# Performance work log

Measured on AMD Instinct MI355X. Metric: run time of the kernel, lower is better.

Reference implementation:

```python
import jax, jax.numpy as jnp
import numpy as np

B = 16384
D = 768           # roberta hidden
SENT = 3          # sentiment features
GRU_IN = D + SENT # 771
H = 128           # memory_dim
FUSION = GRU_IN + H + D  # 1667
E = 7             # num_emotions
S = 65536         # number of (dialog, speaker) memory slots


def setup_inputs() -> dict:
    key = jax.random.key(0)
    ks = jax.random.split(key, 12)
    inp = {
        "h_t": jax.random.normal(ks[0], (B, D), jnp.float32),
        "h_ctx": jax.random.normal(ks[1], (B, D), jnp.float32),
        "sentiment": jax.random.uniform(ks[2], (B, SENT), jnp.float32),
        "slot_ids": jax.random.randint(ks[3], (B,), 0, S, jnp.int32),
        # speaker memory table (gathered/scattered by slot_ids)
        "memory": jax.random.normal(ks[4], (S, H), jnp.float32) * 0.1,
        # GRUCell params (torch layout: rows ordered [r; z; n])
        "W_ih": jax.random.normal(ks[5], (3 * H, GRU_IN), jnp.float32) * 0.02,
        "W_hh": jax.random.normal(ks[6], (3 * H, H), jnp.float32) * 0.02,
        "b_ih": jnp.zeros((3 * H,), jnp.float32),
        "b_hh": jnp.zeros((3 * H,), jnp.float32),
        # heads
        "W_e": jax.random.normal(ks[7], (E, FUSION), jnp.float32) * 0.02,
        "b_e": jnp.zeros((E,), jnp.float32),
        "W_s": jax.random.normal(ks[8], (1, FUSION), jnp.float32) * 0.02,
        "b_s": jnp.zeros((1,), jnp.float32),
    }
    return inp


def _gru_cell(x, h, W_ih, W_hh, b_ih, b_hh):
    # x: [B, GRU_IN], h: [B, H]; torch nn.GRUCell semantics
    gi = x @ W_ih.T + b_ih            # [B, 3H]
    gh = h @ W_hh.T + b_hh            # [B, 3H]
    i_r, i_z, i_n = jnp.split(gi, 3, axis=1)
    h_r, h_z, h_n = jnp.split(gh, 3, axis=1)
    r = jax.nn.sigmoid(i_r + h_r)
    z = jax.nn.sigmoid(i_z + h_z)
    n = jnp.tanh(i_n + r * h_n)
    return (1.0 - z) * n + z * h


def reference(h_t, h_ctx, sentiment, slot_ids, memory, W_ih, W_hh, b_ih, b_hh, W_e, b_e, W_s, b_s):
    h_t_aug = jnp.concatenate([h_t, sentiment], axis=1)      # [B, 771]
    s_t = memory[slot_ids]                                    # gather  [B, H]
    s_new = _gru_cell(h_t_aug, s_t, W_ih, W_hh, b_ih, b_hh)   # [B, H]
    # prediction uses the PRE-update memory s_t (as in the torch loop)
    z_t = jnp.concatenate([h_t_aug, s_t, h_ctx], axis=1)      # [B, 1667] (dropout is identity in eval)
    emotion_logits = z_t @ W_e.T + b_e                        # [B, E]
    shift_logits = (z_t @ W_s.T + b_s)[:, 0]                  # [B]
    # matching the sequential dict updates in the original loop)
    new_memory = memory.at[slot_ids].set(s_new)               # [S, H]
    return emotion_logits, shift_logits, new_memory
```

## Files before the change

### kernel.cpp

```cpp
#include <hip/hip_runtime.h>
#include <hip/hip_bf16.h>

#define B_SZ   16384
#define D_SZ   768
#define H_SZ   128
#define S_SZ   65536
#define E_SZ   7

#define NFR    33
#define NSTEP  53

typedef __attribute__((ext_vector_type(8))) short bf16x8;
typedef __attribute__((ext_vector_type(4))) float f32x4;

#define LD4(p) (*reinterpret_cast<const float4*>(p))
#define MFMA(d, a, b) d = __builtin_amdgcn_mfma_f32_16x16x32_bf16(a, b, d, 0, 0, 0)

#define GLDS(gp, lp) __builtin_amdgcn_global_load_lds(                              \
        (const __attribute__((address_space(1))) unsigned int*)(gp),                \
        (__attribute__((address_space(3))) unsigned int*)(lp), 16, 0, 0)

static __device__ __forceinline__ ushort f2bf(float v) {
    unsigned u = __float_as_uint(v);
    u = (u + 0x7FFFu + ((u >> 16) & 1u)) >> 16;
    return (ushort)u;
}

static __device__ __forceinline__ unsigned pk2(float x, float y) {
    unsigned a = __float_as_uint(x) + 0x8000u;
    unsigned b = __float_as_uint(y) + 0x8000u;
    return __builtin_amdgcn_perm(b, a, 0x07060302);
}

static __device__ __forceinline__ bf16x8 cvt8(float4 a, float4 b) {
    union { unsigned u[4]; bf16x8 v; } r;
    r.u[0] = pk2(a.x, a.y); r.u[1] = pk2(a.z, a.w);
    r.u[2] = pk2(b.x, b.y); r.u[3] = pk2(b.z, b.w);
    return r.v;
}

static __device__ __forceinline__ float w2_value(int n, int k,
    const float* __restrict__ W_ih, const float* __restrict__ W_hh,
    const float* __restrict__ b_ih, const float* __restrict__ b_hh,
    const float* __restrict__ W_e,  const float* __restrict__ b_e,
    const float* __restrict__ W_s,  const float* __restrict__ b_s)
{
    float v = 0.0f;
    if (n < 256) {
        if (k < 768)                        v = W_ih[(size_t)n * 771 + k];
        else if (k < 896)                   v = W_hh[(size_t)n * 128 + (k - 768)];
        else if (k >= 1664 && k < 1667)     v = W_ih[(size_t)n * 771 + 768 + (k - 1664)];
        else if (k == 1667)                 v = b_ih[n] + b_hh[n];
    } else if (n < 384) {
        if (k < 768)                        v = W_ih[(size_t)n * 771 + k];
        else if (k >= 1664 && k < 1667)     v = W_ih[(size_t)n * 771 + 768 + (k - 1664)];
        else if (k == 1667)                 v = b_ih[n];
    } else if (n < 512) {
        int g = n - 128;
        if (k >= 768 && k < 896)            v = W_hh[(size_t)g * 128 + (k - 768)];
        else if (k == 1667)                 v = b_hh[g];
    } else if (n < 520) {
        int e = n - 512;
        const float* Wr = (e < E_SZ) ? (W_e + (size_t)e * 1667) : W_s;
        if (k < 768)                        v = Wr[k];
        else if (k < 896)                   v = Wr[771 + (k - 768)];
        else if (k < 1664)                  v = Wr[899 + (k - 896)];
        else if (k < 1667)                  v = Wr[768 + (k - 1664)];
        else if (k == 1667)                 v = (e < E_SZ) ? b_e[e] : b_s[0];
    }
    return v;
}

__global__ __launch_bounds__(256) void pack_w2f_kernel(
    const float* __restrict__ W_ih, const float* __restrict__ W_hh,
    const float* __restrict__ b_ih, const float* __restrict__ b_hh,
    const float* __restrict__ W_e,  const float* __restrict__ b_e,
    const float* __restrict__ W_s,  const float* __restrict__ b_s,
    ushort* __restrict__ W2f)
{
    int tid = blockIdx.x * 256 + threadIdx.x;
    if (tid >= NFR * NSTEP * 64) return;
    int lane  = tid & 63;
    int kstep = (tid >> 6) % NSTEP;
    int nf    = tid / (NSTEP * 64);
    int n     = nf * 16 + (lane & 15);
    int kbase = kstep * 32 + (lane >> 4) * 8;
    ushort o[8];
#pragma unroll
    for (int j = 0; j < 8; ++j)
        o[j] = f2bf(w2_value(n, kbase + j, W_ih, W_hh, b_ih, b_hh, W_e, b_e, W_s, b_s));
    *reinterpret_cast<uint4*>(W2f + (size_t)tid * 8) = *reinterpret_cast<const uint4*>(o);
}

__global__ __launch_bounds__(256) void winner_kernel(const int* __restrict__ slot_ids,
                                                     int* __restrict__ winner)
{
    int b = blockIdx.x * 256 + threadIdx.x;
    if (b < B_SZ) atomicMax(&winner[slot_ids[b]], b);
}

static __device__ __forceinline__ bf16x8 ldB(const ushort* __restrict__ W2f, int nf, int ks, int lane) {
    return *reinterpret_cast<const bf16x8*>(W2f + ((size_t)(nf * NSTEP + ks) * 64 + lane) * 8);
}

static __device__ __forceinline__ float4 lds_rd(const char* Ab, int st, int row, int h) {
    return *reinterpret_cast<const float4*>(Ab + st * 4096 + row * 128 + ((h ^ (row & 7)) << 4));
}

template<int W>
static __device__ __forceinline__ void chunk_ht8(int c, const char* Ab, int lane,
                                                 const ushort* __restrict__ W2f,
                                                 f32x4* __restrict__ acc, f32x4* __restrict__ hacc)
{
    const int cl = lane & 15, kg = lane >> 4;
#pragma unroll
    for (int st = 0; st < 8; ++st) {
        const int s = c * 8 + st;
        bf16x8 B0 = ldB(W2f, W, s, lane), B1 = ldB(W2f, 8 + W, s, lane), B2 = ldB(W2f, 16 + W, s, lane);
        float4 x0 = lds_rd(Ab, st, cl, 2 * kg), x1 = lds_rd(Ab, st, cl, 2 * kg + 1);
        bf16x8 a0 = cvt8(x0, x1);
        MFMA(acc[0], a0, B0); MFMA(acc[1], a0, B1); MFMA(acc[2], a0, B2);
        float4 y0 = lds_rd(Ab, st, 16 + cl, 2 * kg), y1 = lds_rd(Ab, st, 16 + cl, 2 * kg + 1);
        bf16x8 a1 = cvt8(y0, y1);
        MFMA(acc[4], a1, B0); MFMA(acc[5], a1, B1); MFMA(acc[6], a1, B2);
        if (st == W) {
            bf16x8 Bh = ldB(W2f, 32, s, lane);
            MFMA(hacc[0], a0, Bh); MFMA(hacc[1], a1, Bh);
        }
    }
}

template<int W>
static __device__ __forceinline__ void chunk_c3(const char* Ab, int lane,
                                                const ushort* __restrict__ W2f,
                                                f32x4* __restrict__ acc, f32x4* __restrict__ hacc)
{
    const int cl = lane & 15, kg = lane >> 4;
#pragma unroll
    for (int t = 0; t < 4; ++t) {
        const int s = 24 + t;
        bf16x8 B0 = ldB(W2f, W, s, lane), B1 = ldB(W2f, 8 + W, s, lane), B2 = ldB(W2f, 24 + W, s, lane);
        float4 x0 = lds_rd(Ab, t, cl, 2 * kg), x1 = lds_rd(Ab, t, cl, 2 * kg + 1);
        bf16x8 a0 = cvt8(x0, x1);
        MFMA(acc[0], a0, B0); MFMA(acc[1], a0, B1); MFMA(acc[3], a0, B2);
        float4 y0 = lds_rd(Ab, t, 16 + cl, 2 * kg), y1 = lds_rd(Ab, t, 16 + cl, 2 * kg + 1);
        bf16x8 a1 = cvt8(y0, y1);
        MFMA(acc[4], a1, B0); MFMA(acc[5], a1, B1); MFMA(acc[7], a1, B2);
        if constexpr (W < 4) {
            if (t == W) {
                bf16x8 Bh = ldB(W2f, 32, s, lane);
                MFMA(hacc[0], a0, Bh); MFMA(hacc[1], a1, Bh);
            }
        }
    }
    if constexpr (W >= 4) {
        bf16x8 Bh = ldB(W2f, 32, 24 + W, lane);
        float4 x0 = lds_rd(Ab, W, cl, 2 * kg), x1 = lds_rd(Ab, W, cl, 2 * kg + 1);
        MFMA(hacc[0], cvt8(x0, x1), Bh);
        float4 y0 = lds_rd(Ab, W, 16 + cl, 2 * kg), y1 = lds_rd(Ab, W, 16 + cl, 2 * kg + 1);
        MFMA(hacc[1], cvt8(y0, y1), Bh);
    }
}

template<int W>
static __device__ __forceinline__ void ctx_chunk8(int c, const char* Ab, int lane,
                                                  const ushort* __restrict__ W2f,
                                                  f32x4* __restrict__ hacc)
{
    const int cl = lane & 15, kg = lane >> 4;
    const int s = c * 8 + W;
    bf16x8 Bh = ldB(W2f, 32, s, lane);
    float4 x0 = lds_rd(Ab, W, cl, 2 * kg), x1 = lds_rd(Ab, W, cl, 2 * kg + 1);
    MFMA(hacc[0], cvt8(x0, x1), Bh);
    float4 y0 = lds_rd(Ab, W, 16 + cl, 2 * kg), y1 = lds_rd(Ab, W, 16 + cl, 2 * kg + 1);
    MFMA(hacc[1], cvt8(y0, y1), Bh);
}

template<int W>
static __device__ __forceinline__ void ctx_chunk4(const char* Ab, int lane,
                                                  const ushort* __restrict__ W2f,
                                                  f32x4* __restrict__ hacc)
{
    if constexpr (W < 4) {
        const int cl = lane & 15, kg = lane >> 4;
        bf16x8 Bh = ldB(W2f, 32, 48 + W, lane);
        float4 x0 = lds_rd(Ab, W, cl, 2 * kg), x1 = lds_rd(Ab, W, cl, 2 * kg + 1);
        MFMA(hacc[0], cvt8(x0, x1), Bh);
        float4 y0 = lds_rd(Ab, W, 16 + cl, 2 * kg), y1 = lds_rd(Ab, W, 16 + cl, 2 * kg + 1);
        MFMA(hacc[1], cvt8(y0, y1), Bh);
    }
}

template<int W>
static __device__ __forceinline__ void tail_and_gru(
    const float* __restrict__ sent, const float* __restrict__ memory,
    const int* __restrict__ slot_ids, const int* __restrict__ winner,
    int row0, int lane, const ushort* __restrict__ W2f,
    f32x4* __restrict__ acc, f32x4* __restrict__ hacc, float* __restrict__ out_mem)
{
    const int cl = lane & 15, kg = lane >> 4;
    {
        const int rA0 = row0 + cl, rA1 = rA0 + 16;
        bf16x8 a0, a1;
#pragma unroll
        for (int jj = 0; jj < 8; ++jj) {
            int kk = kg * 8 + jj;
            float v0 = 0.f, v1 = 0.f;
            if (kk < 3)       { v0 = sent[(size_t)rA0 * 3 + kk]; v1 = sent[(size_t)rA1 * 3 + kk]; }
            else if (kk == 3) { v0 = 1.f; v1 = 1.f; }
            a0[jj] = (short)f2bf(v0); a1[jj] = (short)f2bf(v1);
        }
        bf16x8 T0 = ldB(W2f, W, 52, lane),      T1 = ldB(W2f, 8 + W, 52, lane);
        bf16x8 T2 = ldB(W2f, 16 + W, 52, lane), T3 = ldB(W2f, 24 + W, 52, lane);
        MFMA(acc[0], a0, T0); MFMA(acc[1], a0, T1);
        MFMA(acc[2], a0, T2); MFMA(acc[3], a0, T3);
        MFMA(acc[4], a1, T0); MFMA(acc[5], a1, T1);
        MFMA(acc[6], a1, T2); MFMA(acc[7], a1, T3);
        if constexpr (W == 4) {
            bf16x8 Bh = ldB(W2f, 32, 52, lane);
            MFMA(hacc[0], a0, Bh); MFMA(hacc[1], a1, Bh);
        }
    }
    const int j = 16 * W + cl;
#pragma unroll
    for (int rg = 0; rg < 2; ++rg) {
#pragma unroll
        for (int rr = 0; rr < 4; ++rr) {
            const int row  = row0 + rg * 16 + kg * 4 + rr;
            const int slot = slot_ids[row];
            const bool win = (winner[slot] == row);
            float rgate = acc[rg * 4 + 0][rr];
            float zg    = acc[rg * 4 + 1][rr];
            float inn   = acc[rg * 4 + 2][rr];
            float hnn   = acc[rg * 4 + 3][rr];
            rgate = 1.0f / (1.0f + __expf(-rgate));
            zg    = 1.0f / (1.0f + __expf(-zg));
            float nn = tanhf(inn + rgate * hnn);
            float h  = memory[(size_t)slot * H_SZ + j];
            float sn = (1.0f - zg) * nn + zg * h;
            if (win) out_mem[(size_t)slot * H_SZ + j] = sn;
        }
    }
}

__global__ __launch_bounds__(512, 4) void fused_kernel(
    const float* __restrict__ h_t,   const float* __restrict__ h_ctx,
    const float* __restrict__ sent,  const int* __restrict__ slot_ids,
    const float* __restrict__ memory,const ushort* __restrict__ W2f,
    const int* __restrict__ winner,
    float* __restrict__ out_emo, float* __restrict__ out_shift, float* __restrict__ out_mem)
{
    __shared__ alignas(16) char  A_st[2][8 * 4096];
    __shared__ alignas(16) f32x4 redh[8 * 64];

    const int tid  = threadIdx.x;
    const int wave = tid >> 6;
    const int lane = tid & 63;
    const int row0 = blockIdx.x * 32;

    const int st8   = tid & 255;
    const int srow  = st8 >> 3;
    const int scg   = (st8 & 7) ^ (srow & 7);
    const int shalf = tid >> 8;
    const int sslot = slot_ids[row0 + srow];
    const int wb    = (wave & 3) * 1024;

    f32x4 acc[8], hacc[2];
    {
        f32x4 z = {0.f, 0.f, 0.f, 0.f};
#pragma unroll
        for (int i = 0; i < 8; ++i) acc[i] = z;
        hacc[0] = z; hacc[1] = z;
    }

#define STAGE_HT8(BUF, S0) do { _Pragma("unroll")                                         \
    for (int q = 0; q < 4; ++q) { int stp = 2 * q + shalf;                                \
        GLDS(h_t + (size_t)(row0 + srow) * D_SZ + ((S0) + stp) * 32 + scg * 4,            \
             &A_st[BUF][stp * 4096 + wb]); } } while (0)

#define STAGE_MEMCTX(BUF) do { _Pragma("unroll")                                          \
    for (int q = 0; q < 4; ++q) { int stp = 2 * q + shalf;                                \
        if (stp < 4) GLDS(memory + (size_t)sslot * H_SZ + stp * 32 + scg * 4,             \
                          &A_st[BUF][stp * 4096 + wb]);                                   \
        else GLDS(h_ctx + (size_t)(row0 + srow) * D_SZ + (stp - 4) * 32 + scg * 4,        \
                  &A_st[BUF][stp * 4096 + wb]); } } while (0)

#define STAGE_CTX8(BUF, X0) do { _Pragma("unroll")                                        \
    for (int q = 0; q < 4; ++q) { int stp = 2 * q + shalf;                                \
        GLDS(h_ctx + (size_t)(row0 + srow) * D_SZ + ((X0) + stp) * 32 + scg * 4,          \
             &A_st[BUF][stp * 4096 + wb]); } } while (0)

#define STAGE_CTX4(BUF, X0) do { _Pragma("unroll")                                        \
    for (int q = 0; q < 2; ++q) { int stp = 2 * q + shalf;                                \
        GLDS(h_ctx + (size_t)(row0 + srow) * D_SZ + ((X0) + stp) * 32 + scg * 4,          \
             &A_st[BUF][stp * 4096 + wb]); } } while (0)

#define COPYSL(I0, N) do {                                                                \
    for (int k = 0; k < (N); ++k) {                                                       \
        int idx  = ((I0) + k) * 512 + tid;                                                \
        int rr   = idx >> 5;                                                              \
        int c4   = (idx & 31) * 4;                                                        \
        int slot = blockIdx.x * 128 + rr;                                                 \
        if (winner[slot] < 0) {                                                           \
            float4 v = LD4(memory + (size_t)slot * H_SZ + c4);                            \
            *reinterpret_cast<float4*>(out_mem + (size_t)slot * H_SZ + c4) = v;           \
        } } } while (0)

#define BYWAVE(...) do { switch (wave) {                                                  \
    case 0: { constexpr int W = 0; __VA_ARGS__; } break;                                  \
    case 1: { constexpr int W = 1; __VA_ARGS__; } break;                                  \
    case 2: { constexpr int W = 2; __VA_ARGS__; } break;                                  \
    case 3: { constexpr int W = 3; __VA_ARGS__; } break;                                  \
    case 4: { constexpr int W = 4; __VA_ARGS__; } break;                                  \
    case 5: { constexpr int W = 5; __VA_ARGS__; } break;                                  \
    case 6: { constexpr int W = 6; __VA_ARGS__; } break;                                  \
    default:{ constexpr int W = 7; __VA_ARGS__; } break; } } while (0)

    STAGE_HT8(0, 0);
    __syncthreads();

    BYWAVE(chunk_ht8<W>(0, A_st[0], lane, W2f, acc, hacc));
    COPYSL(0, 2);
    STAGE_HT8(1, 8);
    __syncthreads();

    BYWAVE(chunk_ht8<W>(1, A_st[1], lane, W2f, acc, hacc));
    COPYSL(2, 1);
    STAGE_HT8(0, 16);
    __syncthreads();

    BYWAVE(chunk_ht8<W>(2, A_st[0], lane, W2f, acc, hacc));
    COPYSL(3, 1);
    STAGE_MEMCTX(1);
    __syncthreads();

    BYWAVE(chunk_c3<W>(A_st[1], lane, W2f, acc, hacc));
    COPYSL(4, 1);
    STAGE_CTX8(0, 4);
    __syncthreads();

    BYWAVE(ctx_chunk8<W>(4, A_st[0], lane, W2f, hacc));
    COPYSL(5, 1);
    STAGE_CTX8(1, 12);
    __syncthreads();

    BYWAVE(ctx_chunk8<W>(5, A_st[1], lane, W2f, hacc));
    COPYSL(6, 1);
    STAGE_CTX4(0, 20);
    __syncthreads();

    BYWAVE((ctx_chunk4<W>(A_st[0], lane, W2f, hacc),
            tail_and_gru<W>(sent, memory, slot_ids, winner, row0, lane, W2f,
                            acc, hacc, out_mem)));
    COPYSL(7, 1);

#pragma unroll
    for (int rg = 0; rg < 2; ++rg) {
        __syncthreads();
        redh[wave * 64 + lane] = hacc[rg];
        __syncthreads();
        if (tid < 64) {
            f32x4 hv = redh[tid];
#pragma unroll
            for (int w = 1; w < 8; ++w) hv += redh[w * 64 + tid];
            const int col  = tid & 15;
            const int rowb = row0 + rg * 16 + (tid >> 4) * 4;
#pragma unroll
            for (int rr = 0; rr < 4; ++rr) {
                const int row = rowb + rr;
                if (col < E_SZ)       out_emo[(size_t)row * E_SZ + col] = hv[rr];
                else if (col == E_SZ) out_shift[row] = hv[rr];
            }
        }
    }
#undef STAGE_HT8
#undef STAGE_MEMCTX
#undef STAGE_CTX8
#undef STAGE_CTX4
#undef COPYSL
#undef BYWAVE
}

extern "C" void kernel_launch(void* const* d_in, const int* in_sizes, int n_in,
                              void* d_out, int out_size, void* d_ws, size_t ws_size,
                              hipStream_t stream)
{
    const float* h_t     = (const float*)d_in[0];
    const float* h_ctx   = (const float*)d_in[1];
    const float* sent    = (const float*)d_in[2];
    const int*   slot_ids= (const int*)  d_in[3];
    const float* memory  = (const float*)d_in[4];
    const float* W_ih    = (const float*)d_in[5];
    const float* W_hh    = (const float*)d_in[6];
    const float* b_ih    = (const float*)d_in[7];
    const float* b_hh    = (const float*)d_in[8];
    const float* W_e     = (const float*)d_in[9];
    const float* b_e     = (const float*)d_in[10];
    const float* W_s     = (const float*)d_in[11];
    const float* b_s     = (const float*)d_in[12];

    float* out       = (float*)d_out;
    float* out_emo   = out;
    float* out_shift = out + (size_t)B_SZ * E_SZ;
    float* out_mem   = out + (size_t)B_SZ * E_SZ + B_SZ;

    int*    winner = (int*)d_ws;
    ushort* W2f    = (ushort*)((char*)d_ws + (size_t)S_SZ * sizeof(int));

    hipMemsetAsync(winner, 0xFF, (size_t)S_SZ * sizeof(int), stream);

    pack_w2f_kernel<<<(NFR * NSTEP * 64 + 255) / 256, 256, 0, stream>>>(
        W_ih, W_hh, b_ih, b_hh, W_e, b_e, W_s, b_s, W2f);
    winner_kernel<<<B_SZ / 256, 256, 0, stream>>>(slot_ids, winner);
    fused_kernel<<<B_SZ / 32, 512, 0, stream>>>(
        h_t, h_ctx, sent, slot_ids, memory, W2f, winner, out_emo, out_shift, out_mem);
}
```

Measured before the change: 77.16 us.

## Halve rows per block to 16 and raise occupancy target

Each block of the fused kernel now handles 16 batch rows instead of 32, with half the LDS staging buffer, half the accumulators and twice as many blocks. The launch bound is raised to 8 blocks per CU, and the staging, memory-copy and head-reduction index maps are rebuilt to match. The aim is more waves in flight and lower register and LDS pressure per block. In exchange, each weight fragment loaded from global memory now feeds only one MFMA row tile, which doubles weight traffic per row.

```diff
diff --git a/kernel.cpp b/kernel.cpp
--- a/kernel.cpp
+++ b/kernel.cpp
@@ -104,7 +104,7 @@
 }
 
 static __device__ __forceinline__ float4 lds_rd(const char* Ab, int st, int row, int h) {
-    return *reinterpret_cast<const float4*>(Ab + st * 4096 + row * 128 + ((h ^ (row & 7)) << 4));
+    return *reinterpret_cast<const float4*>(Ab + st * 2048 + row * 128 + ((h ^ (row & 7)) << 4));
 }
 
 template<int W>
@@ -120,12 +120,9 @@
         float4 x0 = lds_rd(Ab, st, cl, 2 * kg), x1 = lds_rd(Ab, st, cl, 2 * kg + 1);
         bf16x8 a0 = cvt8(x0, x1);
         MFMA(acc[0], a0, B0); MFMA(acc[1], a0, B1); MFMA(acc[2], a0, B2);
-        float4 y0 = lds_rd(Ab, st, 16 + cl, 2 * kg), y1 = lds_rd(Ab, st, 16 + cl, 2 * kg + 1);
-        bf16x8 a1 = cvt8(y0, y1);
-        MFMA(acc[4], a1, B0); MFMA(acc[5], a1, B1); MFMA(acc[6], a1, B2);
         if (st == W) {
             bf16x8 Bh = ldB(W2f, 32, s, lane);
-            MFMA(hacc[0], a0, Bh); MFMA(hacc[1], a1, Bh);
+            MFMA(hacc[0], a0, Bh);
         }
     }
 }
@@ -143,13 +140,10 @@
         float4 x0 = lds_rd(Ab, t, cl, 2 * kg), x1 = lds_rd(Ab, t, cl, 2 * kg + 1);
         bf16x8 a0 = cvt8(x0, x1);
         MFMA(acc[0], a0, B0); MFMA(acc[1], a0, B1); MFMA(acc[3], a0, B2);
-        float4 y0 = lds_rd(Ab, t, 16 + cl, 2 * kg), y1 = lds_rd(Ab, t, 16 + cl, 2 * kg + 1);
-        bf16x8 a1 = cvt8(y0, y1);
-        MFMA(acc[4], a1, B0); MFMA(acc[5], a1, B1); MFMA(acc[7], a1, B2);
         if constexpr (W < 4) {
             if (t == W) {
                 bf16x8 Bh = ldB(W2f, 32, s, lane);
-                MFMA(hacc[0], a0, Bh); MFMA(hacc[1], a1, Bh);
+                MFMA(hacc[0], a0, Bh);
             }
         }
     }
@@ -157,23 +151,18 @@
         bf16x8 Bh = ldB(W2f, 32, 24 + W, lane);
         float4 x0 = lds_rd(Ab, W, cl, 2 * kg), x1 = lds_rd(Ab, W, cl, 2 * kg + 1);
         MFMA(hacc[0], cvt8(x0, x1), Bh);
-        float4 y0 = lds_rd(Ab, W, 16 + cl, 2 * kg), y1 = lds_rd(Ab, W, 16 + cl, 2 * kg + 1);
-        MFMA(hacc[1], cvt8(y0, y1), Bh);
-    }
-}
-
-template<int W>
-static __device__ __forceinline__ void ctx_chunk8(int c, const char* Ab, int lane,
+    }
+}
+
+template<int W>
+static __device__ __forceinline__ void ctx_chunk8(int sbase, const char* Ab, int lane,
                                                   const ushort* __restrict__ W2f,
                                                   f32x4* __restrict__ hacc)
 {
     const int cl = lane & 15, kg = lane >> 4;
-    const int s = c * 8 + W;
-    bf16x8 Bh = ldB(W2f, 32, s, lane);
+    bf16x8 Bh = ldB(W2f, 32, sbase + W, lane);
     float4 x0 = lds_rd(Ab, W, cl, 2 * kg), x1 = lds_rd(Ab, W, cl, 2 * kg + 1);
     MFMA(hacc[0], cvt8(x0, x1), Bh);
-    float4 y0 = lds_rd(Ab, W, 16 + cl, 2 * kg), y1 = lds_rd(Ab, W, 16 + cl, 2 * kg + 1);
-    MFMA(hacc[1], cvt8(y0, y1), Bh);
 }
 
 template<int W>
@@ -186,8 +175,6 @@
         bf16x8 Bh = ldB(W2f, 32, 48 + W, lane);
         float4 x0 = lds_rd(Ab, W, cl, 2 * kg), x1 = lds_rd(Ab, W, cl, 2 * kg + 1);
         MFMA(hacc[0], cvt8(x0, x1), Bh);
-        float4 y0 = lds_rd(Ab, W, 16 + cl, 2 * kg), y1 = lds_rd(Ab, W, 16 + cl, 2 * kg + 1);
-        MFMA(hacc[1], cvt8(y0, y1), Bh);
     }
 }
 
@@ -200,107 +187,100 @@
 {
     const int cl = lane & 15, kg = lane >> 4;
     {
-        const int rA0 = row0 + cl, rA1 = rA0 + 16;
-        bf16x8 a0, a1;
+        const int rA0 = row0 + cl;
+        bf16x8 a0;
 #pragma unroll
         for (int jj = 0; jj < 8; ++jj) {
             int kk = kg * 8 + jj;
-            float v0 = 0.f, v1 = 0.f;
-            if (kk < 3)       { v0 = sent[(size_t)rA0 * 3 + kk]; v1 = sent[(size_t)rA1 * 3 + kk]; }
-            else if (kk == 3) { v0 = 1.f; v1 = 1.f; }
-            a0[jj] = (short)f2bf(v0); a1[jj] = (short)f2bf(v1);
+            float v0 = 0.f;
+            if (kk < 3)       v0 = sent[(size_t)rA0 * 3 + kk];
+            else if (kk == 3) v0 = 1.f;
+            a0[jj] = (short)f2bf(v0);
         }
         bf16x8 T0 = ldB(W2f, W, 52, lane),      T1 = ldB(W2f, 8 + W, 52, lane);
         bf16x8 T2 = ldB(W2f, 16 + W, 52, lane), T3 = ldB(W2f, 24 + W, 52, lane);
         MFMA(acc[0], a0, T0); MFMA(acc[1], a0, T1);
         MFMA(acc[2], a0, T2); MFMA(acc[3], a0, T3);
-        MFMA(acc[4], a1, T0); MFMA(acc[5], a1, T1);
-        MFMA(acc[6], a1, T2); MFMA(acc[7], a1, T3);
         if constexpr (W == 4) {
             bf16x8 Bh = ldB(W2f, 32, 52, lane);
-            MFMA(hacc[0], a0, Bh); MFMA(hacc[1], a1, Bh);
+            MFMA(hacc[0], a0, Bh);
         }
     }
     const int j = 16 * W + cl;
 #pragma unroll
-    for (int rg = 0; rg < 2; ++rg) {
-#pragma unroll
-        for (int rr = 0; rr < 4; ++rr) {
-            const int row  = row0 + rg * 16 + kg * 4 + rr;
-            const int slot = slot_ids[row];
-            const bool win = (winner[slot] == row);
-            float rgate = acc[rg * 4 + 0][rr];
-            float zg    = acc[rg * 4 + 1][rr];
-            float inn   = acc[rg * 4 + 2][rr];
-            float hnn   = acc[rg * 4 + 3][rr];
-            rgate = 1.0f / (1.0f + __expf(-rgate));
-            zg    = 1.0f / (1.0f + __expf(-zg));
-            float nn = tanhf(inn + rgate * hnn);
-            float h  = memory[(size_t)slot * H_SZ + j];
-            float sn = (1.0f - zg) * nn + zg * h;
-            if (win) out_mem[(size_t)slot * H_SZ + j] = sn;
-        }
-    }
-}
-
-__global__ __launch_bounds__(512, 4) void fused_kernel(
+    for (int rr = 0; rr < 4; ++rr) {
+        const int row  = row0 + kg * 4 + rr;
+        const int slot = slot_ids[row];
+        const bool win = (winner[slot] == row);
+        float rgate = acc[0][rr];
+        float zg    = acc[1][rr];
+        float inn   = acc[2][rr];
+        float hnn   = acc[3][rr];
+        rgate = 1.0f / (1.0f + __expf(-rgate));
+        zg    = 1.0f / (1.0f + __expf(-zg));
+        float nn = tanhf(inn + rgate * hnn);
+        float h  = memory[(size_t)slot * H_SZ + j];
+        float sn = (1.0f - zg) * nn + zg * h;
+        if (win) out_mem[(size_t)slot * H_SZ + j] = sn;
+    }
+}
+
+__global__ __launch_bounds__(512, 8) void fused_kernel(
     const float* __restrict__ h_t,   const float* __restrict__ h_ctx,
     const float* __restrict__ sent,  const int* __restrict__ slot_ids,
     const float* __restrict__ memory,const ushort* __restrict__ W2f,
     const int* __restrict__ winner,
     float* __restrict__ out_emo, float* __restrict__ out_shift, float* __restrict__ out_mem)
 {
-    __shared__ alignas(16) char  A_st[2][8 * 4096];
+    __shared__ alignas(16) char  A_st[2][8 * 2048];
     __shared__ alignas(16) f32x4 redh[8 * 64];
 
     const int tid  = threadIdx.x;
     const int wave = tid >> 6;
     const int lane = tid & 63;
-    const int row0 = blockIdx.x * 32;
-
-    const int st8   = tid & 255;
-    const int srow  = st8 >> 3;
-    const int scg   = (st8 & 7) ^ (srow & 7);
-    const int shalf = tid >> 8;
+    const int row0 = blockIdx.x * 16;
+
+    const int srow  = (tid & 127) >> 3;
+    const int scg   = (lane & 7) ^ (srow & 7);
+    const int sbh   = (wave & 1) * 1024;
+    const int sst0  = wave >> 1;
     const int sslot = slot_ids[row0 + srow];
-    const int wb    = (wave & 3) * 1024;
-
-    f32x4 acc[8], hacc[2];
+
+    f32x4 acc[4], hacc[1];
     {
         f32x4 z = {0.f, 0.f, 0.f, 0.f};
 #pragma unroll
-        for (int i = 0; i < 8; ++i) acc[i] = z;
-        hacc[0] = z; hacc[1] = z;
+        for (int i = 0; i < 4; ++i) acc[i] = z;
+        hacc[0] = z;
     }
 
 #define STAGE_HT8(BUF, S0) do { _Pragma("unroll")                                         \
-    for (int q = 0; q < 4; ++q) { int stp = 2 * q + shalf;                                \
+    for (int rd = 0; rd < 2; ++rd) { int stp = rd * 4 + sst0;                             \
         GLDS(h_t + (size_t)(row0 + srow) * D_SZ + ((S0) + stp) * 32 + scg * 4,            \
-             &A_st[BUF][stp * 4096 + wb]); } } while (0)
+             &A_st[BUF][stp * 2048 + sbh]); } } while (0)
 
 #define STAGE_MEMCTX(BUF) do { _Pragma("unroll")                                          \
-    for (int q = 0; q < 4; ++q) { int stp = 2 * q + shalf;                                \
+    for (int rd = 0; rd < 2; ++rd) { int stp = rd * 4 + sst0;                             \
         if (stp < 4) GLDS(memory + (size_t)sslot * H_SZ + stp * 32 + scg * 4,             \
-                          &A_st[BUF][stp * 4096 + wb]);                                   \
+                          &A_st[BUF][stp * 2048 + sbh]);                                  \
         else GLDS(h_ctx + (size_t)(row0 + srow) * D_SZ + (stp - 4) * 32 + scg * 4,        \
-                  &A_st[BUF][stp * 4096 + wb]); } } while (0)
+                  &A_st[BUF][stp * 2048 + sbh]); } } while (0)
 
 #define STAGE_CTX8(BUF, X0) do { _Pragma("unroll")                                        \
-    for (int q = 0; q < 4; ++q) { int stp = 2 * q + shalf;                                \
+    for (int rd = 0; rd < 2; ++rd) { int stp = rd * 4 + sst0;                             \
         GLDS(h_ctx + (size_t)(row0 + srow) * D_SZ + ((X0) + stp) * 32 + scg * 4,          \
-             &A_st[BUF][stp * 4096 + wb]); } } while (0)
-
-#define STAGE_CTX4(BUF, X0) do { _Pragma("unroll")                                        \
-    for (int q = 0; q < 2; ++q) { int stp = 2 * q + shalf;                                \
+             &A_st[BUF][stp * 2048 + sbh]); } } while (0)
+
+#define STAGE_CTX4(BUF, X0) do { int stp = sst0;                                          \
         GLDS(h_ctx + (size_t)(row0 + srow) * D_SZ + ((X0) + stp) * 32 + scg * 4,          \
-             &A_st[BUF][stp * 4096 + wb]); } } while (0)
+             &A_st[BUF][stp * 2048 + sbh]); } while (0)
 
 #define COPYSL(I0, N) do {                                                                \
     for (int k = 0; k < (N); ++k) {                                                       \
-        int idx  = ((I0) + k) * 512 + tid;                                                \
-        int rr   = idx >> 5;                                                              \
+        int idx  = ((I0) + k) * 512 + tid;                     \
+        int rr   = idx >> 5;                                          \
         int c4   = (idx & 31) * 4;                                                        \
-        int slot = blockIdx.x * 128 + rr;                                                 \
+        int slot = blockIdx.x * 64 + rr;                                                  \
         if (winner[slot] < 0) {                                                           \
             float4 v = LD4(memory + (size_t)slot * H_SZ + c4);                            \
             *reinterpret_cast<float4*>(out_mem + (size_t)slot * H_SZ + c4) = v;           \
@@ -320,57 +300,51 @@
     __syncthreads();
 
     BYWAVE(chunk_ht8<W>(0, A_st[0], lane, W2f, acc, hacc));
-    COPYSL(0, 2);
+    COPYSL(0, 1);
     STAGE_HT8(1, 8);
     __syncthreads();
 
     BYWAVE(chunk_ht8<W>(1, A_st[1], lane, W2f, acc, hacc));
+    COPYSL(1, 1);
+    STAGE_HT8(0, 16);
+    __syncthreads();
+
+    BYWAVE(chunk_ht8<W>(2, A_st[0], lane, W2f, acc, hacc));
     COPYSL(2, 1);
-    STAGE_HT8(0, 16);
-    __syncthreads();
-
-    BYWAVE(chunk_ht8<W>(2, A_st[0], lane, W2f, acc, hacc));
+    STAGE_MEMCTX(1);
+    __syncthreads();
+
+    BYWAVE(chunk_c3<W>(A_st[1], lane, W2f, acc, hacc));
     COPYSL(3, 1);
-    STAGE_MEMCTX(1);
-    __syncthreads();
-
-    BYWAVE(chunk_c3<W>(A_st[1], lane, W2f, acc, hacc));
-    COPYSL(4, 1);
     STAGE_CTX8(0, 4);
     __syncthreads();
 
-    BYWAVE(ctx_chunk8<W>(4, A_st[0], lane, W2f, hacc));
-    COPYSL(5, 1);
+    BYWAVE(ctx_chunk8<W>(32, A_st[0], lane, W2f, hacc));
     STAGE_CTX8(1, 12);
     __syncthreads();
 
-    BYWAVE(ctx_chunk8<W>(5, A_st[1], lane, W2f, hacc));
-    COPYSL(6, 1);
+    BYWAVE(ctx_chunk8<W>(40, A_st[1], lane, W2f, hacc));
     STAGE_CTX4(0, 20);
     __syncthreads();
 
     BYWAVE((ctx_chunk4<W>(A_st[0], lane, W2f, hacc),
             tail_and_gru<W>(sent, memory, slot_ids, winner, row0, lane, W2f,
                             acc, hacc, out_mem)));
-    COPYSL(7, 1);
-
-#pragma unroll
-    for (int rg = 0; rg < 2; ++rg) {
-        __syncthreads();
-        redh[wave * 64 + lane] = hacc[rg];
-        __syncthreads();
-        if (tid < 64) {
-            f32x4 hv = redh[tid];
-#pragma unroll
-            for (int w = 1; w < 8; ++w) hv += redh[w * 64 + tid];
-            const int col  = tid & 15;
-            const int rowb = row0 + rg * 16 + (tid >> 4) * 4;
-#pragma unroll
-            for (int rr = 0; rr < 4; ++rr) {
-                const int row = rowb + rr;
-                if (col < E_SZ)       out_emo[(size_t)row * E_SZ + col] = hv[rr];
-                else if (col == E_SZ) out_shift[row] = hv[rr];
-            }
+
+    __syncthreads();
+    redh[wave * 64 + lane] = hacc[0];
+    __syncthreads();
+    if (tid < 64) {
+        f32x4 hv = redh[tid];
+#pragma unroll
+        for (int w = 1; w < 8; ++w) hv += redh[w * 64 + tid];
+        const int col  = tid & 15;
+        const int rowb = row0 + (tid >> 4) * 4;
+#pragma unroll
+        for (int rr = 0; rr < 4; ++rr) {
+            const int row = rowb + rr;
+            if (col < E_SZ)       out_emo[(size_t)row * E_SZ + col] = hv[rr];
+            else if (col == E_SZ) out_shift[row] = hv[rr];
         }
     }
 #undef STAGE_HT8
@@ -412,6 +386,6 @@
     pack_w2f_kernel<<<(NFR * NSTEP * 64 + 255) / 256, 256, 0, stream>>>(
         W_ih, W_hh, b_ih, b_hh, W_e, b_e, W_s, b_s, W2f);
     winner_kernel<<<B_SZ / 256, 256, 0, stream>>>(slot_ids, winner);
-    fused_kernel<<<B_SZ / 32, 512, 0, stream>>>(
+    fused_kernel<<<B_SZ / 16, 512, 0, stream>>>(
         h_t, h_ctx, sent, slot_ids, memory, W2f, winner, out_emo, out_shift, out_mem);
 }
```

Measured after the change: 75.28 us. -2.4%, faster.
